# Kernel optimization log

Hardware: AMD Instinct MI355X
Metric: run time of the kernel (lower is better)

Reference implementation:

```python
import jax, jax.numpy as jnp
import numpy as np

EPS = 1e-5
GROUPS = 8
OUT_PLANES = 256
GP = OUT_PLANES // GROUPS  # group_planes = 32


def _bn_eval(x, p, ch_axis):
    # p: [4, C] = (gamma, beta, running_mean, running_var); eval-mode batchnorm
    shape = [1] * x.ndim
    shape[ch_axis] = -1
    g, b, m, v = (p[i].reshape(shape) for i in range(4))
    return g * (x - m) * jax.lax.rsqrt(v + EPS) + b


def _make_bn(key, ch):
    k1, k2, k3, k4 = jax.random.split(key, 4)
    gamma = jax.random.uniform(k1, (ch,)) + 0.5
    beta = jax.random.normal(k2, (ch,)) * 0.1
    mean = jax.random.normal(k3, (ch,)) * 0.1
    var = jax.random.uniform(k4, (ch,)) + 0.5
    return jnp.stack([gamma, beta, mean, var])  # [4, ch]


def setup_inputs() -> dict:
    key = jax.random.key(0)
    ks = jax.random.split(key, 6)
    N, C, D, Hh, Ww = 1, 256, 16, 32, 64
    x = jax.random.normal(ks[0], (N, C, D, Hh, Ww), dtype=jnp.float32)
    # qkv 1x1 conv weight: [out_planes*2, in_planes]
    qkv_w = jax.random.normal(ks[1], (OUT_PLANES * 2, C), dtype=jnp.float32) * np.sqrt(1.0 / C)
    # relative positional table: [group_planes*2, 2*H-1]
    relative = jax.random.normal(ks[2], (GP * 2, 2 * Ww - 1), dtype=jnp.float32) * np.sqrt(1.0 / GP)
    bn_qkv = _make_bn(ks[3], OUT_PLANES * 2)
    bn_sim = _make_bn(ks[4], GROUPS * 3)
    bn_out = _make_bn(ks[5], OUT_PLANES * 2)
    return {"x": x, "qkv_w": qkv_w, "relative": relative,
            "bn_qkv": bn_qkv, "bn_sim": bn_sim, "bn_out": bn_out}


def reference(x, qkv_w, relative, bn_qkv, bn_sim, bn_out):
    N, C, D, Hh, Ww = x.shape
    G, OP, gp = GROUPS, OUT_PLANES, GP
    # width == 0: permute(0,2,3,1,4) -> [N, D, Hh, C, Ww]; attend along Ww
    xp = jnp.transpose(x, (0, 2, 3, 1, 4))
    H = Ww
    B = N * D * Hh
    xr = xp.reshape(B, C, H)
    # 1x1 conv + BN over channels
    qkv = jnp.einsum('oc,bch->boh', qkv_w, xr)
    qkv = _bn_eval(qkv, bn_qkv, 1)
    qkv = qkv.reshape(B, G, 2 * gp, H)
    q = qkv[:, :, : gp // 2]          # [B,G,gp/2,H]
    k = qkv[:, :, gp // 2: gp]        # [B,G,gp/2,H]
    v = qkv[:, :, gp:]                # [B,G,gp,H]
    # relative-position gather: emb[c,i,j] = relative[c, i-j+H-1]
    idx = jnp.arange(H)[:, None] - jnp.arange(H)[None, :] + H - 1  # [H,H]
    emb = relative[:, idx]            # [2*gp, H, H]
    q_e = emb[: gp // 2]
    k_e = emb[gp // 2: gp]
    v_e = emb[gp:]
    qr = jnp.einsum('bgci,cij->bgij', q, q_e)
    kr = jnp.einsum('bgci,cij->bgji', k, k_e)  # einsum + transpose(2,3) fused
    qk = jnp.einsum('bgci,bgcj->bgij', q, k)
    sim = jnp.concatenate([qk, qr, kr], axis=1)  # [B, 3G, H, H]
    sim = _bn_eval(sim, bn_sim, 1)
    sim = sim.reshape(B, 3, G, H, H).sum(axis=1)
    sim = jax.nn.softmax(sim, axis=3)
    sv = jnp.einsum('bgij,bgcj->bgci', sim, v)
    sve = jnp.einsum('bgij,cij->bgci', sim, v_e)
    so = jnp.concatenate([sv, sve], axis=-1).reshape(B, 2 * OP, H)
    out = _bn_eval(so, bn_out, 1)
    out = out.reshape(N, D, Hh, OP, 2, H).sum(axis=-2)
    out = jnp.transpose(out, (0, 3, 1, 2, 4))  # [N, OP, D, Hh, Ww]
    return out
```

## Files before the change

kernel.cpp:

```cpp
#include <hip/hip_runtime.h>

#define EPS 1e-5f

typedef _Float16 half4_t __attribute__((ext_vector_type(4)));
typedef _Float16 half8_t __attribute__((ext_vector_type(8)));
typedef float floatx4 __attribute__((ext_vector_type(4)));

__device__ __forceinline__ unsigned short f2hb(float f) {
  _Float16 h = (_Float16)f;
  return __builtin_bit_cast(unsigned short, h);
}
__device__ __forceinline__ float hb2f(unsigned short u) {
  return (float)__builtin_bit_cast(_Float16, u);
}
__device__ __forceinline__ unsigned int pack2(float a, float b) {
  return (unsigned int)f2hb(a) | ((unsigned int)f2hb(b) << 16);
}

#define WS_QKT 33554432
#define WS_RELTQ 50331648
#define WS_RELTK 50335744
#define WS_RELV 50339840
#define WS_BNSF 50348032
#define WS_BNOSC 50348160
#define WS_BNOSH 50350208

__global__ __launch_bounds__(256) void k_qkv_gemm(const float* __restrict__ x,
                                                  const float* __restrict__ W,
                                                  const float* __restrict__ bnq,
                                                  const float* __restrict__ rel,
                                                  const float* __restrict__ bns,
                                                  const float* __restrict__ bno,
                                                  char* __restrict__ ws) {
  unsigned short* qkv_h = (unsigned short*)ws;
  unsigned short* qkT = (unsigned short*)(ws + WS_QKT);
  __shared__ unsigned short Ah[64 * 72];
  __shared__ unsigned short Bh[64 * 66];
  const int tid = threadIdx.x;

  if (blockIdx.x == 0) {
    unsigned short* relTq = (unsigned short*)(ws + WS_RELTQ);
    unsigned short* relTk = (unsigned short*)(ws + WS_RELTK);
    unsigned short* relV = (unsigned short*)(ws + WS_RELV);
    float* bnsF = (float*)(ws + WS_BNSF);
    float* bnoSc = (float*)(ws + WS_BNOSC);
    float* bnoSh = (float*)(ws + WS_BNOSH);
    for (int idx = tid; idx < 2048; idx += 256) {
      const int t = idx >> 4, c = idx & 15;
      relTq[idx] = (t < 127) ? f2hb(rel[c * 127 + t]) : (unsigned short)0;
      relTk[idx] = (t < 127) ? f2hb(rel[(16 + c) * 127 + t]) : (unsigned short)0;
    }
    for (int idx = tid; idx < 4096; idx += 256) {
      const int c = idx >> 7, t = idx & 127;
      relV[idx] = (t < 127) ? f2hb(rel[(32 + c) * 127 + t]) : (unsigned short)0;
    }
    if (tid < 8) {
      const int g = tid;
      const float scA = bns[g] / sqrtf(bns[72 + g] + EPS);
      const float scB = bns[8 + g] / sqrtf(bns[72 + 8 + g] + EPS);
      const float scC = bns[16 + g] / sqrtf(bns[72 + 16 + g] + EPS);
      const float shv = (bns[24 + g] - bns[48 + g] * scA) +
                        (bns[24 + 8 + g] - bns[48 + 8 + g] * scB) +
                        (bns[24 + 16 + g] - bns[48 + 16 + g] * scC);
      bnsF[g * 4 + 0] = scA;
      bnsF[g * 4 + 1] = scB;
      bnsF[g * 4 + 2] = scC;
      bnsF[g * 4 + 3] = shv;
    }
    for (int idx = tid; idx < 512; idx += 256) {
      const float sc = bno[idx] / sqrtf(bno[1536 + idx] + EPS);
      bnoSc[idx] = sc;
      bnoSh[idx] = bno[512 + idx] - bno[1024 + idx] * sc;
    }
  }

  const int raw = blockIdx.x;
  const int xcd = raw & 7;
  const int seq = raw >> 3;
  const int g = seq & 7;
  const int nb_local = seq >> 3;
  const int bidx_n = xcd * 64 + nb_local;
  const int n0 = bidx_n * 64;
  const int o0 = g * 64;
  const size_t b = bidx_n;

  const int lane = tid & 63;
  const int wid = tid >> 6;
  const int wm = (wid >> 1) * 32, wn = (wid & 1) * 32;
  const int l15 = lane & 15, kg = lane >> 4;

  floatx4 acc[2][2] = {};
  const int am = tid >> 2, akq = (tid & 3) * 16;
  const int bk = tid >> 2, bn4 = (tid & 3) * 16;

  for (int ko = 0; ko < 256; ko += 64) {
    __syncthreads();
    {
      unsigned int tp[8];
#pragma unroll
      for (int u = 0; u < 4; ++u) {
        const float4 w4 =
            *reinterpret_cast<const float4*>(&W[(size_t)(o0 + am) * 256 + ko + akq + u * 4]);
        tp[u * 2] = pack2(w4.x, w4.y);
        tp[u * 2 + 1] = pack2(w4.z, w4.w);
      }
      uint4 s0 = {tp[0], tp[1], tp[2], tp[3]};
      uint4 s1 = {tp[4], tp[5], tp[6], tp[7]};
      *reinterpret_cast<uint4*>(&Ah[am * 72 + akq]) = s0;
      *reinterpret_cast<uint4*>(&Ah[am * 72 + akq + 8]) = s1;
    }
    {
#pragma unroll
      for (int u = 0; u < 4; ++u) {
        const float4 x4 =
            *reinterpret_cast<const float4*>(&x[(size_t)(ko + bk) * 32768 + n0 + bn4 + u * 4]);
        uint2 p;
        p.x = pack2(x4.x, x4.y);
        p.y = pack2(x4.z, x4.w);
        *reinterpret_cast<uint2*>(&Bh[bk * 66 + bn4 + u * 4]) = p;
      }
    }
    __syncthreads();
#pragma unroll
    for (int kk = 0; kk < 64; kk += 32) {
      half8_t af[2], bf[2];
#pragma unroll
      for (int fm = 0; fm < 2; ++fm) {
        const int mrow = wm + fm * 16 + l15;
        af[fm] = *reinterpret_cast<const half8_t*>(&Ah[mrow * 72 + kk + kg * 8]);
      }
#pragma unroll
      for (int fn = 0; fn < 2; ++fn) {
        const int ncol = wn + fn * 16 + l15;
        half8_t bv;
#pragma unroll
        for (int e = 0; e < 8; ++e)
          bv[e] = __builtin_bit_cast(_Float16, Bh[(kk + kg * 8 + e) * 66 + ncol]);
        bf[fn] = bv;
      }
#pragma unroll
      for (int fm = 0; fm < 2; ++fm)
#pragma unroll
        for (int fn = 0; fn < 2; ++fn)
          acc[fm][fn] =
              __builtin_amdgcn_mfma_f32_16x16x32_f16(af[fm], bf[fn], acc[fm][fn], 0, 0, 0);
    }
  }

  __syncthreads();
  unsigned short* Tq = Ah;
#pragma unroll
  for (int fm = 0; fm < 2; ++fm) {
    float sc[4], sh[4];
#pragma unroll
    for (int reg = 0; reg < 4; ++reg) {
      const int o = o0 + wm + fm * 16 + kg * 4 + reg;
      sc[reg] = bnq[o] / sqrtf(bnq[1536 + o] + EPS);
      sh[reg] = bnq[512 + o] - bnq[1024 + o] * sc[reg];
    }
#pragma unroll
    for (int fn = 0; fn < 2; ++fn) {
      const int h = wn + fn * 16 + l15;
#pragma unroll
      for (int reg = 0; reg < 4; ++reg) {
        const int row = wm + fm * 16 + kg * 4 + reg;
        const float val = fmaf(acc[fm][fn][reg], sc[reg], sh[reg]);
        if (wm == 0) {
          Tq[(row & 31) * 66 + h] = f2hb(val);
        } else {
          qkv_h[(b * 512 + o0 + row) * 64 + h] = f2hb(val);
        }
      }
    }
  }
  __syncthreads();
  {
    const int h = tid >> 2, c0 = (tid & 3) * 8;
    unsigned short tmp[8];
#pragma unroll
    for (int e = 0; e < 8; ++e) tmp[e] = Tq[(c0 + e) * 66 + h];
    uint4 wv;
    wv.x = (unsigned int)tmp[0] | ((unsigned int)tmp[1] << 16);
    wv.y = (unsigned int)tmp[2] | ((unsigned int)tmp[3] << 16);
    wv.z = (unsigned int)tmp[4] | ((unsigned int)tmp[5] << 16);
    wv.w = (unsigned int)tmp[6] | ((unsigned int)tmp[7] << 16);
    *reinterpret_cast<uint4*>(&qkT[((b * 8 + g) * 64 + h) * 32 + c0]) = wv;
  }
}

#define QKS 36
#define M1S 132
#define PBS 72
#define PPS 136
#define OTS 67

__global__ __launch_bounds__(256, 4) void k_attn(const char* __restrict__ ws,
                                                 float* __restrict__ out) {
  const unsigned short* qkv_h = (const unsigned short*)ws;
  const unsigned short* qkTg = (const unsigned short*)(ws + WS_QKT);
  const unsigned short* relTq = (const unsigned short*)(ws + WS_RELTQ);
  const unsigned short* relTk = (const unsigned short*)(ws + WS_RELTK);
  const unsigned short* relV = (const unsigned short*)(ws + WS_RELV);
  const float* bnsF = (const float*)(ws + WS_BNSF);
  const float* bnoSc = (const float*)(ws + WS_BNOSC);
  const float* bnoSh = (const float*)(ws + WS_BNOSH);

  __shared__ __align__(16) char arena[38400];
  unsigned short* qkL = (unsigned short*)arena;
  unsigned short* M1 = (unsigned short*)(arena + 4608);
  unsigned short* M2 = (unsigned short*)(arena + 21504);
  unsigned short* Pb = (unsigned short*)arena;
  unsigned short* Pp = (unsigned short*)(arena + 9216);
  unsigned short* Vb = (unsigned short*)(arena + 26624);
  float* Sout = (float*)arena;

  const int tid = threadIdx.x;
  const int lane = tid & 63;
  const int wid = tid >> 6;
  const int l15 = lane & 15, kg = lane >> 4;
  const int bg = blockIdx.x;
  const int b = bg >> 3, g = bg & 7;

  {
    const uint4 qv =
        *reinterpret_cast<const uint4*>(&qkTg[(size_t)(((b << 3) + g)) * 2048 + tid * 8]);
    const int i = tid >> 2, c0 = (tid & 3) * 8;
    uint2 lo, hi;
    lo.x = qv.x; lo.y = qv.y; hi.x = qv.z; hi.y = qv.w;
    *reinterpret_cast<uint2*>(&qkL[i * QKS + c0]) = lo;
    *reinterpret_cast<uint2*>(&qkL[i * QKS + c0 + 4]) = hi;
  }
  __syncthreads();

  floatx4 qkreg[4];
  {
    half4_t brq[8], brk[8];
#pragma unroll
    for (int nt = 0; nt < 8; ++nt) {
      brq[nt] = *reinterpret_cast<const half4_t*>(&relTq[(nt * 16 + l15) * 16 + kg * 4]);
      brk[nt] = *reinterpret_cast<const half4_t*>(&relTk[(nt * 16 + l15) * 16 + kg * 4]);
    }
    const half4_t aq = *reinterpret_cast<const half4_t*>(&qkL[(wid * 16 + l15) * QKS + kg * 4]);
    const half4_t ak =
        *reinterpret_cast<const half4_t*>(&qkL[(wid * 16 + l15) * QKS + 16 + kg * 4]);
#pragma unroll
    for (int nt = 0; nt < 4; ++nt) {
      const half4_t bq =
          *reinterpret_cast<const half4_t*>(&qkL[(nt * 16 + l15) * QKS + 16 + kg * 4]);
      const floatx4 z = {};
      qkreg[nt] = __builtin_amdgcn_mfma_f32_16x16x16f16(aq, bq, z, 0, 0, 0);
    }
#pragma unroll
    for (int nt = 0; nt < 8; ++nt) {
      const floatx4 z = {};
      const floatx4 cr = __builtin_amdgcn_mfma_f32_16x16x16f16(aq, brq[nt], z, 0, 0, 0);
#pragma unroll
      for (int r = 0; r < 4; ++r)
        M1[(wid * 16 + kg * 4 + r) * M1S + nt * 16 + l15] = f2hb(cr[r]);
    }
#pragma unroll
    for (int nt = 0; nt < 8; ++nt) {
      const floatx4 z = {};
      const floatx4 cr = __builtin_amdgcn_mfma_f32_16x16x16f16(ak, brk[nt], z, 0, 0, 0);
#pragma unroll
      for (int r = 0; r < 4; ++r)
        M2[(wid * 16 + kg * 4 + r) * M1S + nt * 16 + l15] = f2hb(cr[r]);
    }
  }
  __syncthreads();

  const uint4 vld = *reinterpret_cast<const uint4*>(
      &qkv_h[((size_t)b * 512 + g * 64 + 32 + (tid >> 3)) * 64 + (tid & 7) * 8]);
  float sreg[4][4];
  {
    const float4 bf = *reinterpret_cast<const float4*>(&bnsF[g * 4]);
#pragma unroll
    for (int nt = 0; nt < 4; ++nt) {
      const int j = nt * 16 + l15;
#pragma unroll
      for (int r = 0; r < 4; ++r) {
        const int i = wid * 16 + kg * 4 + r;
        const int d = i - j + 63;
        const float qr = hb2f(M1[i * M1S + d]);
        const float kr = hb2f(M2[j * M1S + 126 - d]);
        sreg[nt][r] = fmaf(bf.x, qkreg[nt][r], fmaf(bf.y, qr, fmaf(bf.z, kr, bf.w)));
      }
    }
  }
  __syncthreads();

  float sm[4];
#pragma unroll
  for (int r = 0; r < 4; ++r) {
    float m = fmaxf(fmaxf(sreg[0][r], sreg[1][r]), fmaxf(sreg[2][r], sreg[3][r]));
    m = fmaxf(m, __shfl_xor(m, 1));
    m = fmaxf(m, __shfl_xor(m, 2));
    m = fmaxf(m, __shfl_xor(m, 4));
    m = fmaxf(m, __shfl_xor(m, 8));
    float s = 0.f;
#pragma unroll
    for (int nt = 0; nt < 4; ++nt) {
      sreg[nt][r] = __expf(sreg[nt][r] - m);
      s += sreg[nt][r];
    }
    s += __shfl_xor(s, 1);
    s += __shfl_xor(s, 2);
    s += __shfl_xor(s, 4);
    s += __shfl_xor(s, 8);
    sm[r] = s;
  }
#pragma unroll
  for (int r = 0; r < 4; ++r) {
    const int i = wid * 16 + kg * 4 + r;
#pragma unroll
    for (int nt = 0; nt < 4; ++nt) {
      const int j = nt * 16 + l15;
      const unsigned short pv = f2hb(sreg[nt][r]);
      Pb[i * PBS + j] = pv;
      Pp[i * PPS + i + 63 - j] = pv;
    }
#pragma unroll
    for (int e = 0; e < 4; ++e) {
      const int z = l15 * 4 + e;
      const int t = (z < i) ? z : z + 64;
      Pp[i * PPS + t] = 0;
    }
  }
  {
    *reinterpret_cast<uint4*>(&Vb[(tid >> 3) * PBS + (tid & 7) * 8]) = vld;
  }
  __syncthreads();

  floatx4 sva[2] = {}, svea[2] = {};
#pragma unroll
  for (int kk = 0; kk < 2; ++kk) {
    const half8_t pa =
        *reinterpret_cast<const half8_t*>(&Pb[(wid * 16 + l15) * PBS + kk * 32 + kg * 8]);
#pragma unroll
    for (int nt = 0; nt < 2; ++nt) {
      const half8_t vb =
          *reinterpret_cast<const half8_t*>(&Vb[(nt * 16 + l15) * PBS + kk * 32 + kg * 8]);
      sva[nt] = __builtin_amdgcn_mfma_f32_16x16x32_f16(pa, vb, sva[nt], 0, 0, 0);
    }
  }
#pragma unroll
  for (int kk = 0; kk < 4; ++kk) {
    const half8_t pp =
        *reinterpret_cast<const half8_t*>(&Pp[(wid * 16 + l15) * PPS + kk * 32 + kg * 8]);
#pragma unroll
    for (int nt = 0; nt < 2; ++nt) {
      const half8_t rb =
          *reinterpret_cast<const half8_t*>(&relV[(nt * 16 + l15) * 128 + kk * 32 + kg * 8]);
      svea[nt] = __builtin_amdgcn_mfma_f32_16x16x32_f16(pp, rb, svea[nt], 0, 0, 0);
    }
  }
  __syncthreads();

#pragma unroll
  for (int nt = 0; nt < 2; ++nt) {
    const int c = nt * 16 + l15;
    const int ch = ((g << 5) + c) * 2;
    const float2 scv = *reinterpret_cast<const float2*>(&bnoSc[ch]);
    const float2 shv = *reinterpret_cast<const float2*>(&bnoSh[ch]);
#pragma unroll
    for (int r = 0; r < 4; ++r) {
      const int i = wid * 16 + kg * 4 + r;
      const float inv = 1.0f / sm[r];
      Sout[c * OTS + i] =
          fmaf(scv.x, sva[nt][r] * inv, shv.x) + fmaf(scv.y, svea[nt][r] * inv, shv.y);
    }
  }
  __syncthreads();
  {
    const size_t outbase = (size_t)b * 64;
#pragma unroll
    for (int r = 0; r < 8; ++r) {
      const int idx = tid + r * 256;
      const int cc = idx >> 6, ii = idx & 63;
      out[(size_t)((g << 5) + cc) * 32768 + outbase + ii] = Sout[cc * OTS + ii];
    }
  }
}

extern "C" void kernel_launch(void* const* d_in, const int* in_sizes, int n_in,
                              void* d_out, int out_size, void* d_ws, size_t ws_size,
                              hipStream_t stream) {
  const float* x = (const float*)d_in[0];
  const float* qkv_w = (const float*)d_in[1];
  const float* relative = (const float*)d_in[2];
  const float* bn_qkv = (const float*)d_in[3];
  const float* bn_sim = (const float*)d_in[4];
  const float* bn_out = (const float*)d_in[5];
  float* out = (float*)d_out;
  char* ws = (char*)d_ws;

  k_qkv_gemm<<<4096, 256, 0, stream>>>(x, qkv_w, bn_qkv, relative, bn_sim, bn_out, ws);
  k_attn<<<4096, 256, 0, stream>>>(ws, out);
}
```

Baseline: 86.74 us.

## Pre-transpose x and W to fp16 in a prep kernel, then run LDS-free QKV GEMM

Adds a prep kernel that converts x to fp16 in a [token, channel] transposed layout and converts W to fp16. This lets the QKV GEMM load MFMA fragments straight from global memory without LDS staging or strided per-element B reads. The GEMM now gives each wave a full 64x64 tile (four batch rows per block, 1024 blocks), and the V part of qkv_h gets a compacted layout. The cost is an extra kernel launch and an extra fp16 round trip of x through global memory.

```diff
diff --git a/kernel.cpp b/kernel.cpp
--- a/kernel.cpp
+++ b/kernel.cpp
@@ -17,28 +17,64 @@
   return (unsigned int)f2hb(a) | ((unsigned int)f2hb(b) << 16);
 }
 
-#define WS_QKT 33554432
-#define WS_RELTQ 50331648
-#define WS_RELTK 50335744
-#define WS_RELV 50339840
-#define WS_BNSF 50348032
-#define WS_BNOSC 50348160
-#define WS_BNOSH 50350208
-
-__global__ __launch_bounds__(256) void k_qkv_gemm(const float* __restrict__ x,
-                                                  const float* __restrict__ W,
-                                                  const float* __restrict__ bnq,
-                                                  const float* __restrict__ rel,
-                                                  const float* __restrict__ bns,
-                                                  const float* __restrict__ bno,
-                                                  char* __restrict__ ws) {
-  unsigned short* qkv_h = (unsigned short*)ws;
-  unsigned short* qkT = (unsigned short*)(ws + WS_QKT);
-  __shared__ unsigned short Ah[64 * 72];
-  __shared__ unsigned short Bh[64 * 66];
-  const int tid = threadIdx.x;
-
-  if (blockIdx.x == 0) {
+#define WS_QKT 16777216
+#define WS_XT 33554432
+#define WS_WH 50331648
+#define WS_RELTQ 50593792
+#define WS_RELTK 50597888
+#define WS_RELV 50601984
+#define WS_BNSF 50610176
+#define WS_BNOSC 50610304
+#define WS_BNOSH 50612352
+
+__global__ __launch_bounds__(256) void k_prep(const float* __restrict__ x,
+                                              const float* __restrict__ W,
+                                              const float* __restrict__ rel,
+                                              const float* __restrict__ bns,
+                                              const float* __restrict__ bno,
+                                              char* __restrict__ ws) {
+  const int bid = blockIdx.x, tid = threadIdx.x;
+  if (bid < 2048) {
+    __shared__ unsigned short Lt[64 * 72];
+    const int k0 = (bid >> 9) * 64;
+    const int n0 = (bid & 511) * 64;
+    {
+      const int kloc = tid >> 2, c0 = (tid & 3) * 16;
+#pragma unroll
+      for (int u = 0; u < 4; ++u) {
+        const float4 v =
+            *reinterpret_cast<const float4*>(&x[(size_t)(k0 + kloc) * 32768 + n0 + c0 + u * 4]);
+        Lt[(c0 + u * 4 + 0) * 72 + kloc] = f2hb(v.x);
+        Lt[(c0 + u * 4 + 1) * 72 + kloc] = f2hb(v.y);
+        Lt[(c0 + u * 4 + 2) * 72 + kloc] = f2hb(v.z);
+        Lt[(c0 + u * 4 + 3) * 72 + kloc] = f2hb(v.w);
+      }
+    }
+    __syncthreads();
+    {
+      unsigned short* xT = (unsigned short*)(ws + WS_XT);
+      const int nloc = tid >> 2, kc = (tid & 3) * 16;
+      const uint4 a = *reinterpret_cast<const uint4*>(&Lt[nloc * 72 + kc]);
+      const uint4 b = *reinterpret_cast<const uint4*>(&Lt[nloc * 72 + kc + 8]);
+      uint4* dst = reinterpret_cast<uint4*>(
+          &((unsigned short*)(ws + WS_XT))[(size_t)(n0 + nloc) * 256 + k0 + kc]);
+      (void)xT;
+      dst[0] = a;
+      dst[1] = b;
+    }
+  } else if (bid < 2056) {
+    unsigned short* Wh = (unsigned short*)(ws + WS_WH);
+    const int base = (bid - 2048) * 16384;
+#pragma unroll
+    for (int u = 0; u < 16; ++u) {
+      const int i = base + u * 1024 + tid * 4;
+      const float4 v = *reinterpret_cast<const float4*>(&W[i]);
+      uint2 p;
+      p.x = pack2(v.x, v.y);
+      p.y = pack2(v.z, v.w);
+      *reinterpret_cast<uint2*>(&Wh[i]) = p;
+    }
+  } else {
     unsigned short* relTq = (unsigned short*)(ws + WS_RELTQ);
     unsigned short* relTk = (unsigned short*)(ws + WS_RELTK);
     unsigned short* relV = (unsigned short*)(ws + WS_RELV);
@@ -73,118 +109,86 @@
       bnoSh[idx] = bno[512 + idx] - bno[1024 + idx] * sc;
     }
   }
-
-  const int raw = blockIdx.x;
-  const int xcd = raw & 7;
-  const int seq = raw >> 3;
-  const int g = seq & 7;
-  const int nb_local = seq >> 3;
-  const int bidx_n = xcd * 64 + nb_local;
-  const int n0 = bidx_n * 64;
-  const int o0 = g * 64;
-  const size_t b = bidx_n;
-
+}
+
+__global__ __launch_bounds__(256) void k_qkv_gemm(const float* __restrict__ bnq,
+                                                  char* __restrict__ ws) {
+  const unsigned short* xT = (const unsigned short*)(ws + WS_XT);
+  const unsigned short* Wh = (const unsigned short*)(ws + WS_WH);
+  unsigned short* qkv_h = (unsigned short*)ws;
+  unsigned short* qkT = (unsigned short*)(ws + WS_QKT);
+  __shared__ unsigned short Tq[4][32 * 72];
+
+  const int tid = threadIdx.x;
   const int lane = tid & 63;
   const int wid = tid >> 6;
-  const int wm = (wid >> 1) * 32, wn = (wid & 1) * 32;
   const int l15 = lane & 15, kg = lane >> 4;
-
-  floatx4 acc[2][2] = {};
-  const int am = tid >> 2, akq = (tid & 3) * 16;
-  const int bk = tid >> 2, bn4 = (tid & 3) * 16;
-
-  for (int ko = 0; ko < 256; ko += 64) {
-    __syncthreads();
-    {
-      unsigned int tp[8];
-#pragma unroll
-      for (int u = 0; u < 4; ++u) {
-        const float4 w4 =
-            *reinterpret_cast<const float4*>(&W[(size_t)(o0 + am) * 256 + ko + akq + u * 4]);
-        tp[u * 2] = pack2(w4.x, w4.y);
-        tp[u * 2 + 1] = pack2(w4.z, w4.w);
-      }
-      uint4 s0 = {tp[0], tp[1], tp[2], tp[3]};
-      uint4 s1 = {tp[4], tp[5], tp[6], tp[7]};
-      *reinterpret_cast<uint4*>(&Ah[am * 72 + akq]) = s0;
-      *reinterpret_cast<uint4*>(&Ah[am * 72 + akq + 8]) = s1;
-    }
-    {
-#pragma unroll
-      for (int u = 0; u < 4; ++u) {
-        const float4 x4 =
-            *reinterpret_cast<const float4*>(&x[(size_t)(ko + bk) * 32768 + n0 + bn4 + u * 4]);
-        uint2 p;
-        p.x = pack2(x4.x, x4.y);
-        p.y = pack2(x4.z, x4.w);
-        *reinterpret_cast<uint2*>(&Bh[bk * 66 + bn4 + u * 4]) = p;
-      }
-    }
-    __syncthreads();
-#pragma unroll
-    for (int kk = 0; kk < 64; kk += 32) {
-      half8_t af[2], bf[2];
-#pragma unroll
-      for (int fm = 0; fm < 2; ++fm) {
-        const int mrow = wm + fm * 16 + l15;
-        af[fm] = *reinterpret_cast<const half8_t*>(&Ah[mrow * 72 + kk + kg * 8]);
-      }
-#pragma unroll
-      for (int fn = 0; fn < 2; ++fn) {
-        const int ncol = wn + fn * 16 + l15;
-        half8_t bv;
-#pragma unroll
-        for (int e = 0; e < 8; ++e)
-          bv[e] = __builtin_bit_cast(_Float16, Bh[(kk + kg * 8 + e) * 66 + ncol]);
-        bf[fn] = bv;
-      }
-#pragma unroll
-      for (int fm = 0; fm < 2; ++fm)
-#pragma unroll
-        for (int fn = 0; fn < 2; ++fn)
-          acc[fm][fn] =
-              __builtin_amdgcn_mfma_f32_16x16x32_f16(af[fm], bf[fn], acc[fm][fn], 0, 0, 0);
-    }
-  }
-
-  __syncthreads();
-  unsigned short* Tq = Ah;
-#pragma unroll
-  for (int fm = 0; fm < 2; ++fm) {
+  const int xcd = blockIdx.x & 7;
+  const int seq = blockIdx.x >> 3;
+  const int g = seq & 7;
+  const int bq = seq >> 3;
+  const size_t bbase = (size_t)(xcd * 16 + bq) * 4;
+  const size_t bb = bbase + wid;
+  const int o0 = g * 64;
+
+  floatx4 acc[4][4] = {};
+  const unsigned short* aBase = Wh + (size_t)(o0 + l15) * 256 + kg * 8;
+  const unsigned short* bBase = xT + (bb * 64 + l15) * 256 + kg * 8;
+
+#pragma unroll
+  for (int kk = 0; kk < 8; ++kk) {
+    half8_t af[4], bf[4];
+#pragma unroll
+    for (int fm = 0; fm < 4; ++fm)
+      af[fm] = *reinterpret_cast<const half8_t*>(aBase + fm * 4096 + kk * 32);
+#pragma unroll
+    for (int fn = 0; fn < 4; ++fn)
+      bf[fn] = *reinterpret_cast<const half8_t*>(bBase + fn * 4096 + kk * 32);
+#pragma unroll
+    for (int fm = 0; fm < 4; ++fm)
+#pragma unroll
+      for (int fn = 0; fn < 4; ++fn)
+        acc[fm][fn] = __builtin_amdgcn_mfma_f32_16x16x32_f16(af[fm], bf[fn], acc[fm][fn], 0, 0, 0);
+  }
+
+#pragma unroll
+  for (int fm = 0; fm < 4; ++fm) {
     float sc[4], sh[4];
 #pragma unroll
     for (int reg = 0; reg < 4; ++reg) {
-      const int o = o0 + wm + fm * 16 + kg * 4 + reg;
+      const int o = o0 + fm * 16 + kg * 4 + reg;
       sc[reg] = bnq[o] / sqrtf(bnq[1536 + o] + EPS);
       sh[reg] = bnq[512 + o] - bnq[1024 + o] * sc[reg];
     }
 #pragma unroll
-    for (int fn = 0; fn < 2; ++fn) {
-      const int h = wn + fn * 16 + l15;
+    for (int fn = 0; fn < 4; ++fn) {
+      const int h = fn * 16 + l15;
 #pragma unroll
       for (int reg = 0; reg < 4; ++reg) {
-        const int row = wm + fm * 16 + kg * 4 + reg;
+        const int row = fm * 16 + kg * 4 + reg;
         const float val = fmaf(acc[fm][fn][reg], sc[reg], sh[reg]);
-        if (wm == 0) {
-          Tq[(row & 31) * 66 + h] = f2hb(val);
+        if (fm < 2) {
+          Tq[wid][row * 72 + h] = f2hb(val);
         } else {
-          qkv_h[(b * 512 + o0 + row) * 64 + h] = f2hb(val);
+          qkv_h[((bb * 8 + g) * 32 + (row - 32)) * 64 + h] = f2hb(val);
         }
       }
     }
   }
   __syncthreads();
-  {
+#pragma unroll
+  for (int t4 = 0; t4 < 4; ++t4) {
+    const size_t btile = bbase + t4;
     const int h = tid >> 2, c0 = (tid & 3) * 8;
     unsigned short tmp[8];
 #pragma unroll
-    for (int e = 0; e < 8; ++e) tmp[e] = Tq[(c0 + e) * 66 + h];
+    for (int e = 0; e < 8; ++e) tmp[e] = Tq[t4][(c0 + e) * 72 + h];
     uint4 wv;
     wv.x = (unsigned int)tmp[0] | ((unsigned int)tmp[1] << 16);
     wv.y = (unsigned int)tmp[2] | ((unsigned int)tmp[3] << 16);
     wv.z = (unsigned int)tmp[4] | ((unsigned int)tmp[5] << 16);
     wv.w = (unsigned int)tmp[6] | ((unsigned int)tmp[7] << 16);
-    *reinterpret_cast<uint4*>(&qkT[((b * 8 + g) * 64 + h) * 32 + c0]) = wv;
+    *reinterpret_cast<uint4*>(&qkT[((btile * 8 + g) * 64 + h) * 32 + c0]) = wv;
   }
 }
 
@@ -270,7 +274,7 @@
   __syncthreads();
 
   const uint4 vld = *reinterpret_cast<const uint4*>(
-      &qkv_h[((size_t)b * 512 + g * 64 + 32 + (tid >> 3)) * 64 + (tid & 7) * 8]);
+      &qkv_h[(((size_t)b * 8 + g) * 32 + (tid >> 3)) * 64 + (tid & 7) * 8]);
   float sreg[4][4];
   {
     const float4 bf = *reinterpret_cast<const float4*>(&bnsF[g * 4]);
@@ -394,6 +398,7 @@
   float* out = (float*)d_out;
   char* ws = (char*)d_ws;
 
-  k_qkv_gemm<<<4096, 256, 0, stream>>>(x, qkv_w, bn_qkv, relative, bn_sim, bn_out, ws);
+  k_prep<<<2057, 256, 0, stream>>>(x, qkv_w, relative, bn_sim, bn_out, ws);
+  k_qkv_gemm<<<1024, 256, 0, stream>>>(bn_qkv, ws);
   k_attn<<<4096, 256, 0, stream>>>(ws, out);
 }
```

Result: slower. 99.99 us (+15.3%).
